# Optimization experiments

Hardware: AMD Instinct MI355X
Metric: run time of the kernel (lower is better)

The kernel has to match this reference:

```python
import jax, jax.numpy as jnp
import numpy as np

H, W, K = 256, 256, 512
Z_THRESHOLD = 3.0
EPS = 1e-8


def setup_inputs() -> dict:
    key = jax.random.key(0)
    k1, k2, k3, k4 = jax.random.split(key, 4)
    # positions uniform in [0,H] x [0,W] x [0,64]
    positions = jax.random.uniform(k1, (K, 3)) * jnp.array([H, W, 64.0], jnp.float32)
    # scales: sigma_x, sigma_y in [1,5]; sigma_z in [0.5,2]
    s_xy = 1.0 + 4.0 * jax.random.uniform(k2, (K, 2))
    s_z = 0.5 + 1.5 * jax.random.uniform(k2, (K, 1))
    scales = jnp.concatenate([s_xy, s_z], axis=-1)
    opacity = jax.random.uniform(k3, (K,))
    intensity = jax.random.uniform(k4, (K,))
    z_target = jnp.array([32.0], jnp.float32)
    return {"positions": positions, "scales": scales, "opacity": opacity,
            "intensity": intensity, "z_target": z_target}


def reference(positions, scales, opacity, intensity, z_target):
    # z culling: instead of boolean gather (data-dependent shape), zero out
    # effective weights of culled Gaussians -> identical math (alpha=0 terms
    # contribute nothing and leave transmittance unchanged).
    z_dist = (z_target - positions[:, 2]) / (scales[:, 2] + EPS)          # (K,)
    z_mask = jnp.abs(z_dist) < Z_THRESHOLD
    z_weight = jnp.exp(-0.5 * z_dist ** 2)
    eff_w = jnp.where(z_mask, opacity * z_weight, 0.0)                    # (K,)

    grid_y = jnp.arange(H, dtype=positions.dtype)[:, None, None]         # (H,1,1)
    grid_x = jnp.arange(W, dtype=positions.dtype)[None, :, None]         # (1,W,1)
    # matches torch: dx pairs row-coord with mu_x, dy pairs col-coord with mu_y
    dxn = (grid_y - positions[:, 0]) / (scales[:, 0] + EPS)               # (H,W,K)
    dyn = (grid_x - positions[:, 1]) / (scales[:, 1] + EPS)               # (H,W,K)
    gauss = jnp.exp(-0.5 * (dxn ** 2 + dyn ** 2))                         # (H,W,K)

    # alpha compositing, sorted by weight descending
    alpha = jnp.clip(gauss * eff_w, 0.0, 0.99)
    order = jnp.argsort(-eff_w)
    alpha = alpha[:, :, order]
    s_int = intensity[order]
    trans = jnp.cumprod(1.0 - alpha, axis=-1)
    trans = jnp.concatenate([jnp.ones_like(trans[:, :, :1]), trans[:, :, :-1]], axis=-1)
    rendered = jnp.sum(trans * alpha * s_int, axis=-1)                    # (H,W)
    return rendered[None]                                                 # (1,H,W)
```

## Files before the change

### kernel.cpp

```cpp
#include <hip/hip_runtime.h>

#define IH 256
#define IW 256
#define NK 512
#define ZTH 3.0f
#define EPSV 1e-8f

#define WS_PX  64
#define WS_PY  (WS_PX + NK)
#define WS_ISY (WS_PY + NK)
#define WS_ISX (WS_ISY + NK)
#define WS_EW  (WS_ISX + NK)
#define WS_IT  (WS_EW + NK)

__launch_bounds__(256, 4)
__global__ void prep_kernel(const float* __restrict__ positions,
                            const float* __restrict__ scales,
                            const float* __restrict__ opacity,
                            const float* __restrict__ intensity,
                            const float* __restrict__ z_target,
                            float* __restrict__ ws) {
    __shared__ float s_w[NK];
    __shared__ int   s_idx[NK];
    __shared__ int   s_cnt;

    const int tid = threadIdx.x;
    const float zt = z_target[0];

    if (tid == 0) s_cnt = 0;
    __syncthreads();

    for (int k = tid; k < NK; k += 256) {
        float pz = positions[3 * k + 2];
        float sz = scales[3 * k + 2];
        float zd = (zt - pz) / (sz + EPSV);
        float w = 0.0f;
        if (fabsf(zd) < ZTH) w = opacity[k] * __expf(-0.5f * zd * zd);
        if (w > 0.0f) {
            int p = atomicAdd(&s_cnt, 1);
            s_w[p] = w;
            s_idx[p] = k;
        }
    }
    __syncthreads();

    const int m = s_cnt;
    int msort = 2;
    while (msort < m) msort <<= 1;

    for (int k = m + tid; k < msort; k += 256) { s_w[k] = -1.0f; s_idx[k] = NK; }

    const int half = msort >> 1;
    for (int size = 2; size <= msort; size <<= 1) {
        for (int stride = size >> 1; stride > 0; stride >>= 1) {
            __syncthreads();
            for (int p = tid; p < half; p += 256) {
                int i = ((p & ~(stride - 1)) << 1) | (p & (stride - 1));
                int j = i | stride;
                bool desc = ((i & size) == 0);
                float wi = s_w[i], wj = s_w[j];
                int   ii = s_idx[i], ij = s_idx[j];
                bool cb_ji = (wj > wi) || (wj == wi && ij < ii);
                bool cb_ij = (wi > wj) || (wi == wj && ii < ij);
                if (desc ? cb_ji : cb_ij) {
                    s_w[i] = wj;  s_w[j] = wi;
                    s_idx[i] = ij; s_idx[j] = ii;
                }
            }
        }
    }
    __syncthreads();

    if (tid == 0) ((int*)ws)[0] = m;
    for (int k = tid; k < m; k += 256) {
        int j = s_idx[k];
        ws[WS_PX  + k] = positions[3 * j + 0];
        ws[WS_PY  + k] = positions[3 * j + 1];
        ws[WS_ISX + k] = 1.0f / (scales[3 * j + 0] + EPSV);
        ws[WS_ISY + k] = 1.0f / (scales[3 * j + 1] + EPSV);
        ws[WS_EW  + k] = s_w[k];
        ws[WS_IT  + k] = intensity[j];
    }
}

__launch_bounds__(256, 4)
__global__ void render_kernel(const float* __restrict__ ws,
                              float* __restrict__ out) {
    __shared__ int   s_n;
    __shared__ float s_py[NK], s_isy[NK], s_rowfac[NK], s_it[NK];

    const int tid = threadIdx.x;
    if (tid == 0) s_n = ((const int*)ws)[0];
    __syncthreads();
    const int n = s_n;

    const float y = (float)blockIdx.x;

    for (int k = tid; k < n; k += 256) {
        float px  = ws[WS_PX + k];
        float isx = ws[WS_ISX + k];
        float dx  = (y - px) * isx;
        s_rowfac[k] = __expf(-0.5f * dx * dx) * ws[WS_EW + k];
        s_py[k]   = ws[WS_PY + k];
        s_isy[k]  = ws[WS_ISY + k];
        s_it[k]   = ws[WS_IT + k];
    }
    __syncthreads();

    const float x = (float)tid;
    float T = 1.0f;
    float acc = 0.0f;
    for (int k = 0; k < n; ++k) {
        float dy = (x - s_py[k]) * s_isy[k];
        float a  = fminf(__expf(-0.5f * dy * dy) * s_rowfac[k], 0.99f);
        acc += T * a * s_it[k];
        T   *= 1.0f - a;
        if (__all(T < 1e-6f)) break;
    }
    out[blockIdx.x * IW + tid] = acc;
}

extern "C" void kernel_launch(void* const* d_in, const int* in_sizes, int n_in,
                              void* d_out, int out_size, void* d_ws, size_t ws_size,
                              hipStream_t stream) {
    (void)in_sizes; (void)n_in; (void)out_size; (void)ws_size;
    const float* positions = (const float*)d_in[0];
    const float* scales    = (const float*)d_in[1];
    const float* opacity   = (const float*)d_in[2];
    const float* intensity = (const float*)d_in[3];
    const float* z_target  = (const float*)d_in[4];
    float* out = (float*)d_out;
    float* ws  = (float*)d_ws;

    hipLaunchKernelGGL(prep_kernel, dim3(1), dim3(256), 0, stream,
                       positions, scales, opacity, intensity, z_target, ws);
    hipLaunchKernelGGL(render_kernel, dim3(IH), dim3(256), 0, stream,
                       ws, out);
}
```

Before: 74.54 us.

## Fuse z-culling sort into render kernel, recompute per block

Replaces the single-block prep kernel plus render kernel with one fused kernel. Every row block now stages all Gaussian inputs in shared memory and redoes the z culling and bitonic sort itself, so the workspace round trip and the serial single-block launch disappear. The cost is that the sort is repeated in all 256 blocks, and shared memory per block grows to roughly 34 KB, which may limit occupancy.

```diff
diff --git a/kernel.cpp b/kernel.cpp
--- a/kernel.cpp
+++ b/kernel.cpp
@@ -6,36 +6,40 @@
 #define ZTH 3.0f
 #define EPSV 1e-8f
 
-#define WS_PX  64
-#define WS_PY  (WS_PX + NK)
-#define WS_ISY (WS_PY + NK)
-#define WS_ISX (WS_ISY + NK)
-#define WS_EW  (WS_ISX + NK)
-#define WS_IT  (WS_EW + NK)
-
 __launch_bounds__(256, 4)
-__global__ void prep_kernel(const float* __restrict__ positions,
-                            const float* __restrict__ scales,
-                            const float* __restrict__ opacity,
-                            const float* __restrict__ intensity,
-                            const float* __restrict__ z_target,
-                            float* __restrict__ ws) {
+__global__ void slice_render_fused(const float* __restrict__ positions,
+                                   const float* __restrict__ scales,
+                                   const float* __restrict__ opacity,
+                                   const float* __restrict__ intensity,
+                                   const float* __restrict__ z_target,
+                                   float* __restrict__ out) {
+    __shared__ float s_pos[3 * NK];
+    __shared__ float s_scl[3 * NK];
+    __shared__ float s_opa[NK];
+    __shared__ float s_int[NK];
     __shared__ float s_w[NK];
     __shared__ int   s_idx[NK];
+    __shared__ float s_py[NK], s_isy[NK], s_rowfac[NK], s_it[NK];
     __shared__ int   s_cnt;
 
     const int tid = threadIdx.x;
     const float zt = z_target[0];
 
+    for (int i = tid; i < 3 * NK; i += 256) {
+        s_pos[i] = positions[i];
+        s_scl[i] = scales[i];
+    }
+    for (int i = tid; i < NK; i += 256) {
+        s_opa[i] = opacity[i];
+        s_int[i] = intensity[i];
+    }
     if (tid == 0) s_cnt = 0;
     __syncthreads();
 
     for (int k = tid; k < NK; k += 256) {
-        float pz = positions[3 * k + 2];
-        float sz = scales[3 * k + 2];
-        float zd = (zt - pz) / (sz + EPSV);
+        float zd = (zt - s_pos[3 * k + 2]) / (s_scl[3 * k + 2] + EPSV);
         float w = 0.0f;
-        if (fabsf(zd) < ZTH) w = opacity[k] * __expf(-0.5f * zd * zd);
+        if (fabsf(zd) < ZTH) w = s_opa[k] * __expf(-0.5f * zd * zd);
         if (w > 0.0f) {
             int p = atomicAdd(&s_cnt, 1);
             s_w[p] = w;
@@ -45,6 +49,8 @@
     __syncthreads();
 
     const int m = s_cnt;
+    if (m == 0) { out[blockIdx.x * IW + tid] = 0.0f; return; }
+
     int msort = 2;
     while (msort < m) msort <<= 1;
 
@@ -71,46 +77,23 @@
     }
     __syncthreads();
 
-    if (tid == 0) ((int*)ws)[0] = m;
+    const float y = (float)blockIdx.x;
     for (int k = tid; k < m; k += 256) {
         int j = s_idx[k];
-        ws[WS_PX  + k] = positions[3 * j + 0];
-        ws[WS_PY  + k] = positions[3 * j + 1];
-        ws[WS_ISX + k] = 1.0f / (scales[3 * j + 0] + EPSV);
-        ws[WS_ISY + k] = 1.0f / (scales[3 * j + 1] + EPSV);
-        ws[WS_EW  + k] = s_w[k];
-        ws[WS_IT  + k] = intensity[j];
-    }
-}
-
-__launch_bounds__(256, 4)
-__global__ void render_kernel(const float* __restrict__ ws,
-                              float* __restrict__ out) {
-    __shared__ int   s_n;
-    __shared__ float s_py[NK], s_isy[NK], s_rowfac[NK], s_it[NK];
-
-    const int tid = threadIdx.x;
-    if (tid == 0) s_n = ((const int*)ws)[0];
-    __syncthreads();
-    const int n = s_n;
-
-    const float y = (float)blockIdx.x;
-
-    for (int k = tid; k < n; k += 256) {
-        float px  = ws[WS_PX + k];
-        float isx = ws[WS_ISX + k];
+        float px  = s_pos[3 * j + 0];
+        float isx = 1.0f / (s_scl[3 * j + 0] + EPSV);
         float dx  = (y - px) * isx;
-        s_rowfac[k] = __expf(-0.5f * dx * dx) * ws[WS_EW + k];
-        s_py[k]   = ws[WS_PY + k];
-        s_isy[k]  = ws[WS_ISY + k];
-        s_it[k]   = ws[WS_IT + k];
+        s_rowfac[k] = __expf(-0.5f * dx * dx) * s_w[k];
+        s_py[k]   = s_pos[3 * j + 1];
+        s_isy[k]  = 1.0f / (s_scl[3 * j + 1] + EPSV);
+        s_it[k]   = s_int[j];
     }
     __syncthreads();
 
     const float x = (float)tid;
     float T = 1.0f;
     float acc = 0.0f;
-    for (int k = 0; k < n; ++k) {
+    for (int k = 0; k < m; ++k) {
         float dy = (x - s_py[k]) * s_isy[k];
         float a  = fminf(__expf(-0.5f * dy * dy) * s_rowfac[k], 0.99f);
         acc += T * a * s_it[k];
@@ -123,17 +106,13 @@
 extern "C" void kernel_launch(void* const* d_in, const int* in_sizes, int n_in,
                               void* d_out, int out_size, void* d_ws, size_t ws_size,
                               hipStream_t stream) {
-    (void)in_sizes; (void)n_in; (void)out_size; (void)ws_size;
+    (void)in_sizes; (void)n_in; (void)out_size; (void)d_ws; (void)ws_size;
     const float* positions = (const float*)d_in[0];
     const float* scales    = (const float*)d_in[1];
     const float* opacity   = (const float*)d_in[2];
     const float* intensity = (const float*)d_in[3];
     const float* z_target  = (const float*)d_in[4];
     float* out = (float*)d_out;
-    float* ws  = (float*)d_ws;
-
-    hipLaunchKernelGGL(prep_kernel, dim3(1), dim3(256), 0, stream,
-                       positions, scales, opacity, intensity, z_target, ws);
-    hipLaunchKernelGGL(render_kernel, dim3(IH), dim3(256), 0, stream,
-                       ws, out);
+    hipLaunchKernelGGL(slice_render_fused, dim3(IH), dim3(256), 0, stream,
+                       positions, scales, opacity, intensity, z_target, out);
 }
```

Measured after the change: 76.54 us. 1.03x slower.
